# Performance work log

Hardware: AMD Instinct MI355X
Metric: run time of the kernel (lower is better)

Reference implementation:

```python
import jax, jax.numpy as jnp
import numpy as np

T, B, E, H = 1024, 4, 1024, 16
Dh = E // H
NEG_INF = float('-inf')


def setup_inputs() -> dict:
    key = jax.random.key(0)
    k1, k2, k3, k4 = jax.random.split(key, 4)
    return {
        'fwd_x': jax.random.normal(k1, (T, B, E), jnp.float32),
        'bwd_x': jax.random.normal(k2, (T, B, E), jnp.float32),
        'in_proj_weight': jax.random.normal(k3, (3 * E, E), jnp.float32) * 0.02,
        'in_proj_bias': jnp.zeros((3 * E,), jnp.float32),
        'out_w': jax.random.normal(k4, (E, E), jnp.float32) * 0.02,
        'out_b': jnp.zeros((E,), jnp.float32),
    }


def reference(fwd_x, bwd_x, in_proj_weight, in_proj_bias, out_w, out_b):
    t, b, e = fwd_x.shape
    s = 2 * t
    dtype = fwd_x.dtype
    zeros = jnp.zeros((1, b, e), dtype)
    # padded_fwd_x[0:t] -> [0, fwd_x[:-1]]; padded_bwd_x[1:t+1] -> [bwd_x[1:], 0]
    q_in = jnp.concatenate([zeros, fwd_x[:-1]], 0) + jnp.concatenate([bwd_x[1:], zeros], 0)
    kv = jnp.concatenate([fwd_x, bwd_x], 0)  # [s, b, e]

    wq, wk, wv = in_proj_weight[:e], in_proj_weight[e:2 * e], in_proj_weight[2 * e:]
    bq, bk, bv = in_proj_bias[:e], in_proj_bias[e:2 * e], in_proj_bias[2 * e:]
    q = (q_in @ wq.T + bq).reshape(t, b, H, Dh)
    k = (kv @ wk.T + bk).reshape(s, b, H, Dh)
    v = (kv @ wv.T + bv).reshape(s, b, H, Dh)

    # NOTE: original module never applies self.scaling in forward -- keep unscaled.
    attn_weights = jnp.einsum('tbhd,sbhd->bhts', q, k)  # [b, H, t, s]

    # mask_curr_state=True: allowed keys are j < i (fwd half) or j > i + t (bwd half)
    i = jnp.arange(t)[:, None]
    j = jnp.arange(s)[None, :]
    allowed = (j >= i + t + 1) | (j <= i - 1)
    mask_bias = jnp.where(allowed, 0.0, NEG_INF).astype(dtype)
    attn_weights = attn_weights + mask_bias[None, None]

    probs = jax.nn.softmax(attn_weights.astype(jnp.float32), axis=-1).astype(dtype)

    attn = jnp.einsum('bhts,sbhd->tbhd', probs, v).reshape(t, b, e)
    attn = attn @ out_w.T + out_b
    avg_weights = probs.mean(axis=1)  # [b, t, s]
    return attn, avg_weights
```

## Files before the change

### kernel.cpp

```cpp
#include <hip/hip_runtime.h>

typedef unsigned short u16;
typedef __attribute__((ext_vector_type(8))) short short8;
typedef __attribute__((ext_vector_type(4))) float f32x4;

#define SM_SHIFT 24.0f

__device__ __forceinline__ u16 f2b(float f) {
  unsigned u = __float_as_uint(f);
  unsigned r = (u + 0x7FFFu + ((u >> 16) & 1u)) >> 16;
  return (u16)r;
}

__device__ __forceinline__ void gload16(const u16* g, u16* l) {
  __builtin_amdgcn_global_load_lds((const __attribute__((address_space(1))) void*)g,
                                   (__attribute__((address_space(3))) void*)l, 16, 0, 0);
}

__device__ __forceinline__ void cast4(const float* __restrict__ src,
                                      u16* __restrict__ dst, int gid) {
  float4 v = *(const float4*)(src + (gid << 2));
  ushort4 o; o.x = f2b(v.x); o.y = f2b(v.y); o.z = f2b(v.z); o.w = f2b(v.w);
  *(ushort4*)(dst + (gid << 2)) = o;
}

__global__ __launch_bounds__(256) void prep_all(const float* __restrict__ fwd,
                                                const float* __restrict__ bwd,
                                                const float* __restrict__ w_in,
                                                const float* __restrict__ w_out,
                                                u16* __restrict__ qin,
                                                u16* __restrict__ kvf,
                                                u16* __restrict__ kvb,
                                                u16* __restrict__ wbf,
                                                u16* __restrict__ wobf) {
  const int blk = blockIdx.x, tid = threadIdx.x;
  if (blk < 4096) {
    int gid = blk * 256 + tid;
    int n = gid >> 8;
    int e4 = (gid & 255) << 2;
    int t = n >> 2, b = n & 3;
    float4 acc = make_float4(0.f, 0.f, 0.f, 0.f);
    if (t > 0) {
      float4 v = *(const float4*)(fwd + (((t - 1) * 4 + b) << 10) + e4);
      acc.x += v.x; acc.y += v.y; acc.z += v.z; acc.w += v.w;
    }
    if (t < 1023) {
      float4 v = *(const float4*)(bwd + (((t + 1) * 4 + b) << 10) + e4);
      acc.x += v.x; acc.y += v.y; acc.z += v.z; acc.w += v.w;
    }
    ushort4 o; o.x = f2b(acc.x); o.y = f2b(acc.y); o.z = f2b(acc.z); o.w = f2b(acc.w);
    *(ushort4*)(qin + (n << 10) + e4) = o;
  } else if (blk < 8192) {
    cast4(fwd, kvf, (blk - 4096) * 256 + tid);
  } else if (blk < 12288) {
    cast4(bwd, kvb, (blk - 8192) * 256 + tid);
  } else if (blk < 15360) {
    cast4(w_in, wbf, (blk - 12288) * 256 + tid);
  } else {
    cast4(w_out, wobf, (blk - 15360) * 256 + tid);
  }
}

template <int MODE, int NB, int MTX, int NTT>
__global__ __launch_bounds__(256) void gemm_bt(const u16* __restrict__ A,
                                               const u16* __restrict__ W,
                                               const float* __restrict__ bias,
                                               void* __restrict__ outp,
                                               void* __restrict__ outp2) {
  __shared__ u16 At[NB][128 * 64];
  __shared__ u16 Wt[NB][128 * 64];
  const int x = blockIdx.x & 7, local = blockIdx.x >> 3;
  const int mt = x * MTX + (local % MTX);
  const int nt = local / MTX;
  const int m0 = mt << 7, n0 = nt << 7;
  const int tid = threadIdx.x;
  const int lane = tid & 63, wid = tid >> 6;
  const int wm = (wid >> 1) << 6, wn = (wid & 1) << 6;
  const int lr = lane & 15, lg = lane >> 4;
  const int srow = lane >> 3, scol = (lane & 7) << 3;
  const int swc = ((lane & 7) ^ srow) << 3;
  f32x4 acc[4][4] = {};
  auto stage = [&](int buf, int k0) {
#pragma unroll
    for (int it = 0; it < 4; it++) {
      int row = (it * 4 + wid) * 8 + srow;
      gload16(&A[(m0 + row) * 1024 + k0 + swc], &At[buf][row * 64 + scol]);
      gload16(&W[(n0 + row) * 1024 + k0 + swc], &Wt[buf][row * 64 + scol]);
    }
  };
  auto compute = [&](int buf) {
#pragma unroll
    for (int kk = 0; kk < 64; kk += 32) {
      short8 af[4], bf[4];
#pragma unroll
      for (int i = 0; i < 4; i++) {
        int co = (((kk >> 3) + lg) ^ (lr & 7)) << 3;
        af[i] = *(const short8*)&At[buf][(wm + i * 16 + lr) * 64 + co];
        bf[i] = *(const short8*)&Wt[buf][(wn + i * 16 + lr) * 64 + co];
      }
#pragma unroll
      for (int i = 0; i < 4; i++)
#pragma unroll
        for (int j = 0; j < 4; j++)
          acc[i][j] = __builtin_amdgcn_mfma_f32_16x16x32_bf16(af[i], bf[j], acc[i][j], 0, 0, 0);
    }
  };
  if constexpr (NB == 2) {
    stage(0, 0);
    __syncthreads();
    for (int step = 0; step < 16; ++step) {
      const int cur = step & 1;
      if (step < 15) stage(cur ^ 1, (step + 1) << 6);
      compute(cur);
      __syncthreads();
    }
  } else {
    for (int step = 0; step < 16; ++step) {
      __syncthreads();
      stage(0, step << 6);
      __syncthreads();
      compute(0);
    }
  }
#pragma unroll
  for (int i = 0; i < 4; i++) {
#pragma unroll
    for (int j = 0; j < 4; j++) {
      int n = n0 + wn + j * 16 + lr;
      float bv = bias[n];
#pragma unroll
      for (int r = 0; r < 4; r++) {
        int m = m0 + wm + i * 16 + lg * 4 + r;
        float v = acc[i][j][r] + bv;
        if (MODE == 3) {
          ((float*)outp)[m * 1024 + n] = v;
        } else if (MODE == 0) {
          int tb = m & 3, ts = m >> 2, hh = n >> 6, d = n & 63;
          ((u16*)outp)[((tb * 16 + hh) * 1024 + ts) * 64 + d] = f2b(v);
        } else {
          u16* ob = (n0 < 1024) ? (u16*)outp : (u16*)outp2;
          int nl = (n0 < 1024) ? n : n - 1024;
          int tb = m & 3, ts = m >> 2, hh = nl >> 6, d = nl & 63;
          ob[((tb * 16 + hh) * 2048 + ts) * 64 + d] = f2b(v);
        }
      }
    }
  }
}

__global__ __launch_bounds__(256) void transpose_v(const u16* __restrict__ v,
                                                   u16* __restrict__ vt) {
  __shared__ u16 L[64 * 66];
  const int blk = blockIdx.x;
  const int bh = blk >> 5, s0 = (blk & 31) << 6;
  const int tid = threadIdx.x;
  const u16* src = v + ((size_t)bh * 2048 + s0) * 64;
  u16* dst = vt + (size_t)bh * 64 * 2048 + s0;
#pragma unroll
  for (int it = 0; it < 2; ++it) {
    int idx = it * 256 + tid;
    int sl = idx >> 3, dc = (idx & 7) << 3;
    short8 v8 = *(const short8*)&src[sl * 64 + dc];
#pragma unroll
    for (int e = 0; e < 8; ++e)
      L[(dc + e) * 66 + sl] = (u16)v8[e];
  }
  __syncthreads();
#pragma unroll
  for (int it = 0; it < 2; ++it) {
    int idx = it * 256 + tid;
    int dr = idx >> 3, sc = (idx & 7) << 3;
    *(short8*)&dst[(size_t)dr * 2048 + sc] = *(const short8*)&L[dr * 66 + sc];
  }
}

__global__ __launch_bounds__(256) void attn_fwd(const u16* __restrict__ qb,
                                                const u16* __restrict__ kb,
                                                const u16* __restrict__ vtb,
                                                u16* __restrict__ attn_bf,
                                                float* __restrict__ st_il) {
  __shared__ u16 Kt[64 * 64];
  __shared__ u16 Vt[64 * 64];
  __shared__ u16 Pt[4][16 * 72];
  const int g = blockIdx.x;
  const int L = ((g & 7) << 7) | (g >> 3);
  const int t0 = (L & 15) << 6;
  const int h = (L >> 4) & 15;
  const int b = L >> 8;
  const int tid = threadIdx.x, lane = tid & 63, w = tid >> 6;
  const int lr = lane & 15, lg = lane >> 4;
  const int bh = b * 16 + h;
  const int sw0 = ((lg ^ (lr & 7)) << 3);
  const int sw1 = sw0 ^ 32;
  const u16* qrow = qb + ((bh << 10) + t0 + (w << 4) + lr) * 64;
  short8 qf0 = *(const short8*)&qrow[lg * 8];
  short8 qf1 = *(const short8*)&qrow[32 + lg * 8];
  const u16* kbase = kb + (size_t)(bh << 11) * 64;
  const u16* vbase = vtb + (size_t)(bh << 6) * 2048;
  f32x4 acc[4] = {};
  f32x4 accl = {};
  const int n1 = (t0 >> 6) + 1;
  const int grow = lane >> 3, gcol = (lane & 7) << 3;
  short8 ones;
#pragma unroll
  for (int j = 0; j < 8; ++j) ones[j] = (short)0x3F80;
  for (int ti = 0; ti < 17; ++ti) {
    const int s0 = (ti < n1) ? (ti << 6) : (t0 + 1024 + ((ti - n1) << 6));
    __syncthreads();
#pragma unroll
    for (int it = 0; it < 2; ++it) {
      int row = (it * 4 + w) * 8 + grow;
      int swc = (((lane & 7) ^ (row & 7)) << 3);
      gload16(&kbase[(size_t)(s0 + row) * 64 + swc], &Kt[row * 64 + gcol]);
      gload16(&vbase[(size_t)row * 2048 + s0 + swc], &Vt[row * 64 + gcol]);
    }
    __syncthreads();
    float pv[4][4];
#pragma unroll
    for (int c = 0; c < 4; c++) {
      f32x4 sc = {};
      short8 kf0 = *(const short8*)&Kt[(c * 16 + lr) * 64 + sw0];
      short8 kf1 = *(const short8*)&Kt[(c * 16 + lr) * 64 + sw1];
      sc = __builtin_amdgcn_mfma_f32_16x16x32_bf16(qf0, kf0, sc, 0, 0, 0);
      sc = __builtin_amdgcn_mfma_f32_16x16x32_bf16(qf1, kf1, sc, 0, 0, 0);
      int j = s0 + c * 16 + lr;
#pragma unroll
      for (int r = 0; r < 4; r++) {
        int i = t0 + (w << 4) + lg * 4 + r;
        float e = __expf(sc[r] - SM_SHIFT);
        pv[c][r] = ((j < i) || (j > i + 1024)) ? e : 0.f;
      }
    }
#pragma unroll
    for (int c = 0; c < 4; c++)
#pragma unroll
      for (int r = 0; r < 4; r++)
        Pt[w][(lg * 4 + r) * 72 + c * 16 + lr] = f2b(pv[c][r]);
    short8 pf0 = *(const short8*)&Pt[w][lr * 72 + lg * 8];
    short8 pf1 = *(const short8*)&Pt[w][lr * 72 + 32 + lg * 8];
    accl = __builtin_amdgcn_mfma_f32_16x16x32_bf16(pf0, ones, accl, 0, 0, 0);
    accl = __builtin_amdgcn_mfma_f32_16x16x32_bf16(pf1, ones, accl, 0, 0, 0);
#pragma unroll
    for (int dd = 0; dd < 4; dd++) {
      short8 vf0 = *(const short8*)&Vt[(dd * 16 + lr) * 64 + sw0];
      short8 vf1 = *(const short8*)&Vt[(dd * 16 + lr) * 64 + sw1];
      acc[dd] = __builtin_amdgcn_mfma_f32_16x16x32_bf16(pf0, vf0, acc[dd], 0, 0, 0);
      acc[dd] = __builtin_amdgcn_mfma_f32_16x16x32_bf16(pf1, vf1, acc[dd], 0, 0, 0);
    }
  }
  float inv[4];
#pragma unroll
  for (int r = 0; r < 4; r++) inv[r] = 1.f / accl[r];
  const int trow = t0 + (w << 4) + lg * 4;
#pragma unroll
  for (int dd = 0; dd < 4; dd++)
#pragma unroll
    for (int r = 0; r < 4; r++)
      attn_bf[((trow + r) * 4 + b) * 1024 + h * 64 + dd * 16 + lr] = f2b(acc[dd][r] * inv[r]);
#pragma unroll
  for (int r = 0; r < 4; r++)
    if (lr == r)
      st_il[(bh << 10) + trow + r] = inv[r];
}

__global__ __launch_bounds__(256) void attn_avg(const u16* __restrict__ qb,
                                                const u16* __restrict__ kb,
                                                const float* __restrict__ st_il,
                                                float* __restrict__ avg) {
  __shared__ u16 Kt[2][128 * 64];
  __shared__ float Si[16][64];
  const int g = blockIdx.x;
  const int L = ((g & 7) << 7) | (g >> 3);
  const int s0 = (L & 15) << 7;
  const int t0 = ((L >> 4) & 15) << 6;
  const int b = L >> 8;
  const int tid = threadIdx.x, lane = tid & 63, w = tid >> 6;
  const int lr = lane & 15, lg = lane >> 4;
  const int trow = t0 + (w << 4) + lg * 4;
  float* obase = avg + (size_t)b * (1024 * 2048);
  if ((s0 > t0 + 62) && (s0 + 127 < t0 + 1025)) {
#pragma unroll
    for (int c = 0; c < 8; c++)
#pragma unroll
      for (int r = 0; r < 4; r++)
        obase[(trow + r) * 2048 + s0 + c * 16 + lr] = 0.f;
    return;
  }
  for (int i = tid; i < 1024; i += 256) {
    int hh = i >> 6, tt = i & 63;
    Si[hh][tt] = st_il[(((b << 4) + hh) << 10) + t0 + tt];
  }
  const int sw0 = ((lg ^ (lr & 7)) << 3);
  const int sw1 = sw0 ^ 32;
  const int grow = lane >> 3, gcol = (lane & 7) << 3;
  const int srr = (w << 4) + lg * 4;
  auto stage = [&](int buf, int hh) {
    const u16* kb_h = kb + ((size_t)(((b << 4) + hh) << 11) + s0) * 64;
#pragma unroll
    for (int it = 0; it < 4; ++it) {
      int row = (it * 4 + w) * 8 + grow;
      int swc = (((lane & 7) ^ (row & 7)) << 3);
      gload16(&kb_h[(size_t)row * 64 + swc], &Kt[buf][row * 64 + gcol]);
    }
  };
  stage(0, 0);
  __syncthreads();
  float accv[8][4] = {};
  for (int h = 0; h < 16; h++) {
    const int cur = h & 1;
    if (h < 15) stage(cur ^ 1, h + 1);
    const int bh = (b << 4) + h;
    const u16* qrow = qb + ((bh << 10) + t0 + (w << 4) + lr) * 64;
    short8 qf0 = *(const short8*)&qrow[lg * 8];
    short8 qf1 = *(const short8*)&qrow[32 + lg * 8];
    float ih[4];
#pragma unroll
    for (int r = 0; r < 4; r++) ih[r] = Si[h][srr + r];
#pragma unroll
    for (int c = 0; c < 8; c++) {
      int c0 = s0 + (c << 4);
      if (c0 >= t0 + 63 && c0 <= t0 + 1009) continue;
      f32x4 sc = {};
      short8 kf0 = *(const short8*)&Kt[cur][(c * 16 + lr) * 64 + sw0];
      short8 kf1 = *(const short8*)&Kt[cur][(c * 16 + lr) * 64 + sw1];
      sc = __builtin_amdgcn_mfma_f32_16x16x32_bf16(qf0, kf0, sc, 0, 0, 0);
      sc = __builtin_amdgcn_mfma_f32_16x16x32_bf16(qf1, kf1, sc, 0, 0, 0);
      int j = c0 + lr;
#pragma unroll
      for (int r = 0; r < 4; r++) {
        int i = t0 + (w << 4) + lg * 4 + r;
        if ((j < i) || (j > i + 1024))
          accv[c][r] += __expf(sc[r] - SM_SHIFT) * ih[r];
      }
    }
    __syncthreads();
  }
#pragma unroll
  for (int c = 0; c < 8; c++)
#pragma unroll
    for (int r = 0; r < 4; r++)
      obase[(trow + r) * 2048 + s0 + c * 16 + lr] = accv[c][r] * 0.0625f;
}

extern "C" void kernel_launch(void* const* d_in, const int* in_sizes, int n_in,
                              void* d_out, int out_size, void* d_ws, size_t ws_size,
                              hipStream_t stream) {
  const float* fwd   = (const float*)d_in[0];
  const float* bwd   = (const float*)d_in[1];
  const float* w_in  = (const float*)d_in[2];
  const float* b_in  = (const float*)d_in[3];
  const float* w_out = (const float*)d_in[4];
  const float* b_out = (const float*)d_in[5];

  char* ws = (char*)d_ws;
  u16*  q_in_bf = (u16*)(ws);
  u16*  kv_bf   = (u16*)(ws + 8388608);
  u16*  vt_bf   = (u16*)(ws + 8388608);
  u16*  w_bf    = (u16*)(ws + 25165824);
  u16*  wo_bf   = (u16*)(ws + 31457280);
  u16*  q_bf    = (u16*)(ws + 33554432);
  u16*  k_bf    = (u16*)(ws + 41943040);
  u16*  v_tmp   = (u16*)(ws + 58720256);
  u16*  attn_bf = (u16*)(ws + 75497472);
  float* st_il  = (float*)(ws + 83886080);

  float* out_attn = (float*)d_out;
  float* out_avg  = (float*)d_out + 4194304;

  prep_all<<<16384, 256, 0, stream>>>(fwd, bwd, w_in, w_out, q_in_bf, kv_bf,
                                      kv_bf + 4194304, w_bf, wo_bf);

  gemm_bt<0, 2, 4, 8><<<256, 256, 0, stream>>>(q_in_bf, w_bf, b_in,
                                               (void*)q_bf, nullptr);
  gemm_bt<1, 1, 8, 16><<<1024, 256, 0, stream>>>(kv_bf, w_bf + 1048576,
                                                 b_in + 1024, (void*)k_bf,
                                                 (void*)v_tmp);
  transpose_v<<<2048, 256, 0, stream>>>(v_tmp, vt_bf);

  attn_fwd<<<1024, 256, 0, stream>>>(q_bf, k_bf, vt_bf, attn_bf, st_il);

  gemm_bt<3, 2, 4, 8><<<256, 256, 0, stream>>>(attn_bf, wo_bf, b_out,
                                               (void*)out_attn, nullptr);

  attn_avg<<<1024, 256, 0, stream>>>(q_bf, k_bf, st_il, out_avg);
}
```

Measured before the change: 201.9 us.

## Use 256x256-tile double-buffered KV projection GEMM with LDS-staged coalesced stores

```diff
diff --git a/kernel.cpp b/kernel.cpp
--- a/kernel.cpp
+++ b/kernel.cpp
@@ -61,14 +61,101 @@
   }
 }
 
-template <int MODE, int NB, int MTX, int NTT>
+__global__ __launch_bounds__(512, 2) void gemm_kv256(const u16* __restrict__ A,
+                                                     const u16* __restrict__ W,
+                                                     const float* __restrict__ bias,
+                                                     u16* __restrict__ outK,
+                                                     u16* __restrict__ outV) {
+  __shared__ u16 SH[65536];
+  const int x = blockIdx.x & 7, local = blockIdx.x >> 3;
+  const int mt = x * 4 + (local & 3);
+  const int nt = local >> 2;
+  const int m0 = mt << 8, n0 = nt << 8;
+  const int tid = threadIdx.x;
+  const int lane = tid & 63, wid = tid >> 6;
+  const int wm = (wid >> 2) << 7;
+  const int wn = (wid & 3) << 6;
+  const int lr = lane & 15, lg = lane >> 4;
+  const int scol = (lane & 7) << 3;
+  const int swc = ((lane & 7) ^ (lane >> 3)) << 3;
+  f32x4 acc[8][4] = {};
+  auto At = [&](int buf) { return SH + buf * 16384; };
+  auto Wt = [&](int buf) { return SH + 32768 + buf * 16384; };
+  auto stage = [&](int buf, int k0) {
+    u16* a = At(buf); u16* w = Wt(buf);
+#pragma unroll
+    for (int it = 0; it < 4; it++) {
+      int row = (it * 8 + wid) * 8 + (lane >> 3);
+      gload16(&A[(size_t)(m0 + row) * 1024 + k0 + swc], &a[row * 64 + scol]);
+      gload16(&W[(size_t)(n0 + row) * 1024 + k0 + swc], &w[row * 64 + scol]);
+    }
+  };
+  auto compute = [&](int buf) {
+    const u16* a = At(buf); const u16* w = Wt(buf);
+#pragma unroll
+    for (int kk = 0; kk < 64; kk += 32) {
+      int co = (((kk >> 3) + lg) ^ (lr & 7)) << 3;
+      short8 af[8], bf[4];
+#pragma unroll
+      for (int i = 0; i < 8; i++)
+        af[i] = *(const short8*)&a[(wm + i * 16 + lr) * 64 + co];
+#pragma unroll
+      for (int j = 0; j < 4; j++)
+        bf[j] = *(const short8*)&w[(wn + j * 16 + lr) * 64 + co];
+#pragma unroll
+      for (int i = 0; i < 8; i++)
+#pragma unroll
+        for (int j = 0; j < 4; j++)
+          acc[i][j] = __builtin_amdgcn_mfma_f32_16x16x32_bf16(af[i], bf[j], acc[i][j], 0, 0, 0);
+    }
+  };
+  stage(0, 0);
+  __syncthreads();
+  for (int step = 0; step < 16; ++step) {
+    const int cur = step & 1;
+    if (step < 15) stage(cur ^ 1, (step + 1) << 6);
+    compute(cur);
+    __syncthreads();
+  }
+  u16* C = SH;
+#pragma unroll
+  for (int i = 0; i < 8; i++) {
+#pragma unroll
+    for (int j = 0; j < 4; j++) {
+      int n = wn + j * 16 + lr;
+      float bv = bias[n0 + n];
+      int np = n ^ (lg << 4);
+#pragma unroll
+      for (int r = 0; r < 4; r++) {
+        int m = wm + i * 16 + lg * 4 + r;
+        C[m * 256 + np] = f2b(acc[i][j][r] + bv);
+      }
+    }
+  }
+  __syncthreads();
+  const bool isK = (n0 < 1024);
+  u16* ob = isK ? outK : outV;
+  const int hbase = isK ? (n0 >> 6) : ((n0 - 1024) >> 6);
+  const int ts0 = m0 >> 2;
+  const int ts = tid >> 3, c8d = tid & 7;
+#pragma unroll
+  for (int k = 0; k < 16; ++k) {
+    int tb = k >> 2, hh = k & 3;
+    int m = ts * 4 + tb;
+    int c8 = (hh * 8 + c8d) ^ ((ts & 3) << 1);
+    uint4 val = *(const uint4*)&C[m * 256 + c8 * 8];
+    size_t off = ((size_t)(tb * 16 + hbase + hh) * 2048 + ts0 + ts) * 64 + c8d * 8;
+    *(uint4*)&ob[off] = val;
+  }
+}
+
+template <int MODE, int MTX>
 __global__ __launch_bounds__(256) void gemm_bt(const u16* __restrict__ A,
                                                const u16* __restrict__ W,
                                                const float* __restrict__ bias,
-                                               void* __restrict__ outp,
-                                               void* __restrict__ outp2) {
-  __shared__ u16 At[NB][128 * 64];
-  __shared__ u16 Wt[NB][128 * 64];
+                                               void* __restrict__ outp) {
+  __shared__ u16 At[2][128 * 64];
+  __shared__ u16 Wt[2][128 * 64];
   const int x = blockIdx.x & 7, local = blockIdx.x >> 3;
   const int mt = x * MTX + (local % MTX);
   const int nt = local / MTX;
@@ -105,22 +192,13 @@
           acc[i][j] = __builtin_amdgcn_mfma_f32_16x16x32_bf16(af[i], bf[j], acc[i][j], 0, 0, 0);
     }
   };
-  if constexpr (NB == 2) {
-    stage(0, 0);
+  stage(0, 0);
+  __syncthreads();
+  for (int step = 0; step < 16; ++step) {
+    const int cur = step & 1;
+    if (step < 15) stage(cur ^ 1, (step + 1) << 6);
+    compute(cur);
     __syncthreads();
-    for (int step = 0; step < 16; ++step) {
-      const int cur = step & 1;
-      if (step < 15) stage(cur ^ 1, (step + 1) << 6);
-      compute(cur);
-      __syncthreads();
-    }
-  } else {
-    for (int step = 0; step < 16; ++step) {
-      __syncthreads();
-      stage(0, step << 6);
-      __syncthreads();
-      compute(0);
-    }
   }
 #pragma unroll
   for (int i = 0; i < 4; i++) {
@@ -134,14 +212,9 @@
         float v = acc[i][j][r] + bv;
         if (MODE == 3) {
           ((float*)outp)[m * 1024 + n] = v;
-        } else if (MODE == 0) {
+        } else {
           int tb = m & 3, ts = m >> 2, hh = n >> 6, d = n & 63;
           ((u16*)outp)[((tb * 16 + hh) * 1024 + ts) * 64 + d] = f2b(v);
-        } else {
-          u16* ob = (n0 < 1024) ? (u16*)outp : (u16*)outp2;
-          int nl = (n0 < 1024) ? n : n - 1024;
-          int tb = m & 3, ts = m >> 2, hh = nl >> 6, d = nl & 63;
-          ob[((tb * 16 + hh) * 2048 + ts) * 64 + d] = f2b(v);
         }
       }
     }
@@ -370,17 +443,15 @@
   prep_all<<<16384, 256, 0, stream>>>(fwd, bwd, w_in, w_out, q_in_bf, kv_bf,
                                       kv_bf + 4194304, w_bf, wo_bf);
 
-  gemm_bt<0, 2, 4, 8><<<256, 256, 0, stream>>>(q_in_bf, w_bf, b_in,
-                                               (void*)q_bf, nullptr);
-  gemm_bt<1, 1, 8, 16><<<1024, 256, 0, stream>>>(kv_bf, w_bf + 1048576,
-                                                 b_in + 1024, (void*)k_bf,
-                                                 (void*)v_tmp);
+  gemm_bt<0, 4><<<256, 256, 0, stream>>>(q_in_bf, w_bf, b_in, (void*)q_bf);
+  gemm_kv256<<<256, 512, 0, stream>>>(kv_bf, w_bf + 1048576, b_in + 1024,
+                                      k_bf, v_tmp);
   transpose_v<<<2048, 256, 0, stream>>>(v_tmp, vt_bf);
 
   attn_fwd<<<1024, 256, 0, stream>>>(q_bf, k_bf, vt_bf, attn_bf, st_il);
 
-  gemm_bt<3, 2, 4, 8><<<256, 256, 0, stream>>>(attn_bf, wo_bf, b_out,
-                                               (void*)out_attn, nullptr);
+  gemm_bt<3, 4><<<256, 256, 0, stream>>>(attn_bf, wo_bf, b_out,
+                                         (void*)out_attn);
 
   attn_avg<<<1024, 256, 0, stream>>>(q_bf, k_bf, st_il, out_avg);
 }
```

After: 190.6 us. 5.6% less time.
